# Kernel tuning notes

Hardware: AMD Instinct MI355X
Metric: run time of the kernel (lower is better)

The kernel has to match this reference:

```python
import jax, jax.numpy as jnp
import numpy as np

C = 64
CR = C // 8  # reduced channels for Q/K


def _conv1x1(x, W, b):
    # 1x1 conv == per-pixel linear over channels: x [b,c,h,w], W [o,c], b [o]
    return jnp.einsum('bchw,oc->bohw', x, W) + b[None, :, None, None]


def setup_inputs() -> dict:
    key = jax.random.key(0)
    ks = jax.random.split(key, 12)
    b, c, h, w = 8, C, 48, 48
    s = 1.0 / np.sqrt(c)
    inp = {
        'x1': jax.random.normal(ks[0], (b, c, h, w), jnp.float32),
        'x2': jax.random.normal(ks[1], (b, c, h, w), jnp.float32),
        'Wqk1': jax.random.normal(ks[2], (2 * CR, c), jnp.float32) * s,
        'bqk1': jnp.zeros((2 * CR,), jnp.float32),
        'Wqk2': jax.random.normal(ks[3], (2 * CR, c), jnp.float32) * s,
        'bqk2': jnp.zeros((2 * CR,), jnp.float32),
        'Wv1': jax.random.normal(ks[4], (c, c), jnp.float32) * s,
        'bv1': jnp.zeros((c,), jnp.float32),
        'Wv2': jax.random.normal(ks[5], (c, c), jnp.float32) * s,
        'bv2': jnp.zeros((c,), jnp.float32),
        'gamma': jnp.zeros((1,), jnp.float32) + 0.1,  # nonzero so output depends on attn
        'beta': jnp.zeros((1,), jnp.float32) + 0.1,
    }
    return inp


def reference(x1, x2, Wqk1, bqk1, Wqk2, bqk2, Wv1, bv1, Wv2, bv2, gamma, beta):
    b, c, h, w = x1.shape
    n = h * w
    qk1 = _conv1x1(x1, Wqk1, bqk1)
    qk2 = _conv1x1(x2, Wqk2, bqk2)
    q1, k1 = qk1[:, :CR], qk1[:, CR:]
    q2, k2 = qk2[:, :CR], qk2[:, CR:]
    # flatten spatial: [b, cr, n]
    q1 = q1.reshape(b, CR, n); k1 = k1.reshape(b, CR, n)
    q2 = q2.reshape(b, CR, n); k2 = k2.reshape(b, CR, n)
    v1 = _conv1x1(x1, Wv1, bv1).reshape(b, c, n)
    v2 = _conv1x1(x2, Wv2, bv2).reshape(b, c, n)
    # attn[b,i,j] = softmax_j( q[:, :, i] . k[:, :, j] )
    attn1 = jax.nn.softmax(jnp.einsum('bci,bcj->bij', q1, k1), axis=-1)
    attn2 = jax.nn.softmax(jnp.einsum('bci,bcj->bij', q2, k2), axis=-1)
    # out[:, :, j] = sum_i v[:, :, i] * attn[:, i, j]
    o1 = jnp.einsum('bci,bij->bcj', v1, attn2).reshape(b, c, h, w) * gamma + x1
    o2 = jnp.einsum('bci,bij->bcj', v2, attn1).reshape(b, c, h, w) * beta + x2
    return (o1, o2)
```

## Files before the change

kernel.cpp:

```cpp
#include <hip/hip_runtime.h>
#include <hip/hip_bf16.h>

#define NB   8
#define CCH  64
#define CR8  8
#define NPX  2304
#define BCN  (NB*CCH*NPX)
#define LOG2E 1.4426950408889634f

typedef short  short8   __attribute__((ext_vector_type(8)));
typedef unsigned short ushort4t __attribute__((ext_vector_type(4)));
typedef unsigned short ushort8t __attribute__((ext_vector_type(8)));
typedef float  float4t  __attribute__((ext_vector_type(4)));
typedef float  float16t __attribute__((ext_vector_type(16)));

static __device__ __forceinline__ unsigned short bf16bits(float f) {
    __hip_bfloat16 hb = __float2bfloat16(f);
    return *(unsigned short*)&hb;
}

#define WS_QB1 0
#define WS_KB1 (WS_QB1 + 147456)
#define WS_QB2 (WS_KB1 + 147456)
#define WS_KB2 (WS_QB2 + 147456)
#define WS_V1  (WS_KB2 + 147456)
#define WS_V2  (WS_V1 + BCN/2)
#define WS_PD  (WS_V2 + BCN/2)

__global__ __launch_bounds__(256) void proj_kernel(
    const float* __restrict__ x1, const float* __restrict__ x2,
    const float* __restrict__ Wqk1, const float* __restrict__ bqk1,
    const float* __restrict__ Wqk2, const float* __restrict__ bqk2,
    const float* __restrict__ Wv1,  const float* __restrict__ bv1,
    const float* __restrict__ Wv2,  const float* __restrict__ bv2,
    float* __restrict__ ws, float* __restrict__ out)
{
    const int t    = threadIdx.x;
    const int lane = t & 63;
    const int w    = t >> 6;
    const int n16  = lane & 15;
    const int c4   = lane >> 4;
    const int nt   = w & 1;
    const int mh   = w >> 1;
    const int b    = blockIdx.y;
    const int px   = blockIdx.x * 32 + nt * 16 + n16;

    const float* xsb[2];
    xsb[0] = x1 + ((size_t)b * CCH) * NPX + px;
    xsb[1] = x2 + ((size_t)b * CCH) * NPX + px;

    float xr[2][16];
    short8 bfrag[2][2];
    #pragma unroll
    for (int st = 0; st < 2; st++) {
        #pragma unroll
        for (int ch = 0; ch < 2; ch++) {
            #pragma unroll
            for (int j = 0; j < 8; j++)
                xr[st][ch * 8 + j] = xsb[st][(ch * 32 + c4 * 8 + j) * NPX];
            short8 f;
            #pragma unroll
            for (int j = 0; j < 8; j++)
                f[j] = (short)bf16bits(xr[st][ch * 8 + j]);
            bfrag[st][ch] = f;
        }
    }

    if (mh == 0) {
        #pragma unroll
        for (int st = 0; st < 2; st++) {
            float* outs = out + (st ? (size_t)BCN : 0);
            #pragma unroll
            for (int e = 0; e < 16; e++) {
                const int ch = (e >> 3) * 32 + c4 * 8 + (e & 7);
                outs[((size_t)b * CCH + ch) * NPX + px] = xr[st][e];
            }
        }
    }

    float4t acc[5];
    #pragma unroll
    for (int mt = 0; mt < 5; mt++) { acc[mt][0]=0.f; acc[mt][1]=0.f; acc[mt][2]=0.f; acc[mt][3]=0.f; }

    #pragma unroll
    for (int mt = 0; mt < 5; mt++) {
        const int mi  = mh * 5 + mt;
        const int isqk = (mi < 2);
        const int st  = isqk ? (mi & 1) : (mi >= 6);
        const float* Wb;
        int rowbase;
        if (isqk) { Wb = (mi == 0) ? Wqk1 : Wqk2; rowbase = 0; }
        else      { Wb = (mi >= 6) ? Wv2 : Wv1; rowbase = (mi - (mi >= 6 ? 6 : 2)) * 16; }
        const float* wrow = Wb + (size_t)(rowbase + n16) * 64 + c4 * 8;

        const short8 bf0 = st ? bfrag[1][0] : bfrag[0][0];
        const short8 bf1 = st ? bfrag[1][1] : bfrag[0][1];

        #pragma unroll
        for (int ch = 0; ch < 2; ch++) {
            const float4 a0 = *(const float4*)(wrow + ch * 32);
            const float4 a1 = *(const float4*)(wrow + ch * 32 + 4);
            short8 af;
            af[0] = (short)bf16bits(a0.x); af[1] = (short)bf16bits(a0.y);
            af[2] = (short)bf16bits(a0.z); af[3] = (short)bf16bits(a0.w);
            af[4] = (short)bf16bits(a1.x); af[5] = (short)bf16bits(a1.y);
            af[6] = (short)bf16bits(a1.z); af[7] = (short)bf16bits(a1.w);
            acc[mt] = __builtin_amdgcn_mfma_f32_16x16x32_bf16(
                af, ch ? bf1 : bf0, acc[mt], 0, 0, 0);
        }
    }

    #pragma unroll
    for (int mt = 0; mt < 5; mt++) {
        const int mi = mh * 5 + mt;
        if (mi < 2) {
            const int st = mi & 1;
            const float* bqk = st ? bqk2 : bqk1;
            unsigned short* qb = (unsigned short*)(ws + (st ? WS_QB2 : WS_QB1));
            unsigned short* kb = (unsigned short*)(ws + (st ? WS_KB2 : WS_KB1));
            const size_t rbase = (size_t)(b * NPX + px) * 16;
            #pragma unroll
            for (int r = 0; r < 4; r++) {
                const int oc = c4 * 4 + r;
                const float val = acc[mt][r] + bqk[oc];
                if (oc < 8)
                    qb[rbase + oc] = bf16bits(val * LOG2E);
                else
                    kb[rbase + (oc - 8)] = bf16bits(val);
            }
            ushort8t zq, zk;
            #pragma unroll
            for (int e = 0; e < 8; e++) { zq[e] = 0; zk[e] = 0; }
            zk[0] = 0x3F80; zk[1] = 0x3F80;
            if (c4 == 0) *(ushort8t*)(qb + rbase + 8) = zq;
            if (c4 == 2) *(ushort8t*)(kb + rbase + 8) = zk;
        } else {
            const int st = (mi >= 6);
            const int vt_ = mi - (st ? 6 : 2);
            const float* bv = st ? bv2 : bv1;
            unsigned short* v = (unsigned short*)(ws + (st ? WS_V2 : WS_V1));
            #pragma unroll
            for (int r = 0; r < 4; r++) {
                const int oc = vt_ * 16 + c4 * 4 + r;
                const float val = acc[mt][r] + bv[oc];
                v[((size_t)b * CCH + oc) * NPX + px] = bf16bits(val);
            }
        }
    }
}

__global__ __launch_bounds__(256) void stats_kernel(float* __restrict__ ws)
{
    const int t  = threadIdx.x;
    const int w  = t >> 6;
    const int n  = t & 31;
    const int h  = (t & 63) >> 5;
    const int jsb = blockIdx.x;
    const int iq  = blockIdx.y;
    const int ab  = blockIdx.z;
    const int b   = ab & 7;
    const int a   = ab >> 3;

    const unsigned short* qb = (const unsigned short*)(ws + (a ? WS_QB2 : WS_QB1));
    const unsigned short* kb = (const unsigned short*)(ws + (a ? WS_KB2 : WS_KB1));
    float* pd = ws + WS_PD;

    __shared__ float red[4][576];

    const int j = jsb * 128 + w * 32 + n;
    const short8 kfrag = *(const short8*)(kb + (size_t)(b * NPX + j) * 16 + h * 8);

    for (int ib = 0; ib < 18; ib++) {
        const int i = iq * 576 + ib * 32 + n;
        const short8 qfrag = *(const short8*)(qb + (size_t)(b * NPX + i) * 16 + h * 8);
        float16t acc = {};
        acc = __builtin_amdgcn_mfma_f32_32x32x16_bf16(kfrag, qfrag, acc, 0, 0, 0);
        float s0 = 0.f, s1 = 0.f, s2 = 0.f, s3 = 0.f;
        #pragma unroll
        for (int r = 0; r < 4; r++) {
            s0 += exp2f(acc[4 * r + 0]);
            s1 += exp2f(acc[4 * r + 1]);
            s2 += exp2f(acc[4 * r + 2]);
            s3 += exp2f(acc[4 * r + 3]);
        }
        float ssum = (s0 + s1) + (s2 + s3);
        ssum += __shfl_xor(ssum, 32);
        if (h == 0) red[w][ib * 32 + n] = ssum;
    }
    __syncthreads();
    for (int idx = t; idx < 576; idx += 256)
        pd[((size_t)ab * 18 + jsb) * NPX + iq * 576 + idx] =
            red[0][idx] + red[1][idx] + red[2][idx] + red[3][idx];
}

__global__ __launch_bounds__(256) void merge_fold(float* __restrict__ ws)
{
    const float* pd = ws + WS_PD;
    const int idx = blockIdx.x * 256 + threadIdx.x;
    const int i  = idx % NPX;
    const int ab = idx / NPX;
    const int b  = ab & 7;
    const int a  = ab >> 3;
    float d = 0.f;
    #pragma unroll
    for (int c = 0; c < 18; c++)
        d += pd[((size_t)ab * 18 + c) * NPX + i];
    const float m = -__log2f(d);

    const unsigned short mh = bf16bits(m);
    __hip_bfloat16 hb; *(unsigned short*)&hb = mh;
    const unsigned short ml = bf16bits(m - __bfloat162float(hb));

    unsigned short* qb = (unsigned short*)(ws + (a ? WS_QB2 : WS_QB1));
    const size_t rbase = (size_t)(b * NPX + i) * 16;
    qb[rbase + 8] = mh;
    qb[rbase + 9] = ml;
}

__global__ __launch_bounds__(256) void out_kernel(
    const float* __restrict__ gamma, const float* __restrict__ beta,
    const float* __restrict__ ws, float* __restrict__ out)
{
    const int t  = threadIdx.x;
    const int jt = blockIdx.x;
    const int b  = blockIdx.y;
    const int z  = blockIdx.z;
    const int o  = z >> 1;
    const int ihalf = z & 1;

    const int a = o ? 0 : 1;
    const unsigned short* qb = (const unsigned short*)(ws + (a ? WS_QB2 : WS_QB1));
    const unsigned short* kb = (const unsigned short*)(ws + (a ? WS_KB2 : WS_KB1));
    const unsigned short* v  = (const unsigned short*)(ws + (o ? WS_V2 : WS_V1));
    const float  scale = o ? beta[0] : gamma[0];

    __shared__ unsigned short vt[64][72];
    __shared__ unsigned short pt[64][132];

    const int j0   = jt * 64;
    const int lane = t & 63;
    const int w    = t >> 6;
    const int n    = lane & 31;
    const int h    = lane >> 5;
    const int jh   = w & 1;
    const int ihq  = w >> 1;
    const int cbase = 32 * (w & 1);
    const int jbase = 32 * (w >> 1);

    const short8 kfrag = *(const short8*)(kb + (size_t)(b * NPX + j0 + 32 * jh + n) * 16 + h * 8);

    float16t oacc = {};

    for (int it = 0; it < 18; it++) {
        const int i0 = ihalf * 1152 + it * 64;
        __syncthreads();

        #pragma unroll
        for (int r = 0; r < 2; r++) {
            const int seg = t + r * 256;
            const int c = seg >> 3, s8 = seg & 7;
            *(float4*)&vt[c][s8 * 8] =
                *(const float4*)(v + ((size_t)b * CCH + c) * NPX + i0 + s8 * 8);
        }

        const short8 qfrag = *(const short8*)(qb + (size_t)(b * NPX + i0 + 32 * ihq + n) * 16 + h * 8);
        float16t sc = {};
        sc = __builtin_amdgcn_mfma_f32_32x32x16_bf16(qfrag, kfrag, sc, 0, 0, 0);

        #pragma unroll
        for (int gq = 0; gq < 4; gq++) {
            const int ibl = 32 * ihq + 8 * gq + 4 * h;
            ushort4t pk;
            pk[0] = bf16bits(exp2f(sc[gq * 4 + 0]));
            pk[1] = bf16bits(exp2f(sc[gq * 4 + 1]));
            pk[2] = bf16bits(exp2f(sc[gq * 4 + 2]));
            pk[3] = bf16bits(exp2f(sc[gq * 4 + 3]));
            *(ushort4t*)&pt[32 * jh + n][ibl] = pk;
        }
        __syncthreads();

        #pragma unroll
        for (int kk = 0; kk < 4; kk++) {
            const short8 afrag = *(const short8*)&vt[cbase + n][kk * 16 + h * 8];
            const short8 bfrag = *(const short8*)&pt[jbase + n][kk * 16 + h * 8];
            oacc = __builtin_amdgcn_mfma_f32_32x32x16_bf16(afrag, bfrag, oacc, 0, 0, 0);
        }
    }

    const size_t outoff = o ? (size_t)BCN : 0;
    #pragma unroll
    for (int r = 0; r < 16; r++) {
        const int row = (r & 3) + 8 * (r >> 2) + 4 * h;
        const int c = cbase + row;
        const size_t gidx = ((size_t)b * CCH + c) * NPX + j0 + jbase + n;
        atomicAdd(&out[outoff + gidx], oacc[r] * scale);
    }
}

extern "C" void kernel_launch(void* const* d_in, const int* in_sizes, int n_in,
                              void* d_out, int out_size, void* d_ws, size_t ws_size,
                              hipStream_t stream)
{
    const float* x1   = (const float*)d_in[0];
    const float* x2   = (const float*)d_in[1];
    const float* Wqk1 = (const float*)d_in[2];
    const float* bqk1 = (const float*)d_in[3];
    const float* Wqk2 = (const float*)d_in[4];
    const float* bqk2 = (const float*)d_in[5];
    const float* Wv1  = (const float*)d_in[6];
    const float* bv1  = (const float*)d_in[7];
    const float* Wv2  = (const float*)d_in[8];
    const float* bv2  = (const float*)d_in[9];
    const float* gamma = (const float*)d_in[10];
    const float* beta  = (const float*)d_in[11];
    float* out = (float*)d_out;
    float* ws  = (float*)d_ws;

    proj_kernel<<<dim3(72, 8), 256, 0, stream>>>(
        x1, x2, Wqk1, bqk1, Wqk2, bqk2, Wv1, bv1, Wv2, bv2, ws, out);
    stats_kernel<<<dim3(18, 4, 16), 256, 0, stream>>>(ws);
    merge_fold<<<dim3(144), 256, 0, stream>>>(ws);
    out_kernel<<<dim3(36, 8, 4), 256, 0, stream>>>(gamma, beta, ws, out);
}
```

Measured before the change: 164.1 us.

## Prefetch next tiles in stats/out kernels and split out_kernel i-range into quarters

Software-pipelines the global loads in both stats_kernel (next Q fragment) and out_kernel (next V tile and Q fragment) into registers one iteration ahead, so load latency overlaps with MFMA and exp work. It also splits out_kernel's i-dimension into four chunks instead of two, doubling the grid to raise occupancy and parallelism on the many CUs. The cost is more atomicAdd traffic to the output and higher register pressure from the prefetch buffers.

After: 154.8 us. 5.6% less time.

```diff
diff --git a/kernel.cpp b/kernel.cpp
--- a/kernel.cpp
+++ b/kernel.cpp
@@ -170,11 +170,16 @@
     const int j = jsb * 128 + w * 32 + n;
     const short8 kfrag = *(const short8*)(kb + (size_t)(b * NPX + j) * 16 + h * 8);
 
+    short8 qf = *(const short8*)(qb + (size_t)(b * NPX + iq * 576 + n) * 16 + h * 8);
+
     for (int ib = 0; ib < 18; ib++) {
-        const int i = iq * 576 + ib * 32 + n;
-        const short8 qfrag = *(const short8*)(qb + (size_t)(b * NPX + i) * 16 + h * 8);
+        short8 qn = qf;
+        if (ib + 1 < 18) {
+            const int i = iq * 576 + (ib + 1) * 32 + n;
+            qn = *(const short8*)(qb + (size_t)(b * NPX + i) * 16 + h * 8);
+        }
         float16t acc = {};
-        acc = __builtin_amdgcn_mfma_f32_32x32x16_bf16(kfrag, qfrag, acc, 0, 0, 0);
+        acc = __builtin_amdgcn_mfma_f32_32x32x16_bf16(kfrag, qf, acc, 0, 0, 0);
         float s0 = 0.f, s1 = 0.f, s2 = 0.f, s3 = 0.f;
         #pragma unroll
         for (int r = 0; r < 4; r++) {
@@ -186,6 +191,7 @@
         float ssum = (s0 + s1) + (s2 + s3);
         ssum += __shfl_xor(ssum, 32);
         if (h == 0) red[w][ib * 32 + n] = ssum;
+        qf = qn;
     }
     __syncthreads();
     for (int idx = t; idx < 576; idx += 256)
@@ -225,8 +231,8 @@
     const int jt = blockIdx.x;
     const int b  = blockIdx.y;
     const int z  = blockIdx.z;
-    const int o  = z >> 1;
-    const int ihalf = z & 1;
+    const int o  = z >> 2;
+    const int ihalf = z & 3;
 
     const int a = o ? 0 : 1;
     const unsigned short* qb = (const unsigned short*)(ws + (a ? WS_QB2 : WS_QB1));
@@ -249,23 +255,35 @@
 
     const short8 kfrag = *(const short8*)(kb + (size_t)(b * NPX + j0 + 32 * jh + n) * 16 + h * 8);
 
+    const int c0 = t >> 3, s80 = (t & 7) * 8;
+    const int c1 = (t + 256) >> 3, s81 = ((t + 256) & 7) * 8;
+
+    const int ibase = ihalf * 576;
+    float4 vpre0 = *(const float4*)(v + ((size_t)b * CCH + c0) * NPX + ibase + s80);
+    float4 vpre1 = *(const float4*)(v + ((size_t)b * CCH + c1) * NPX + ibase + s81);
+    short8 qpre  = *(const short8*)(qb + (size_t)(b * NPX + ibase + 32 * ihq + n) * 16 + h * 8);
+
     float16t oacc = {};
 
-    for (int it = 0; it < 18; it++) {
-        const int i0 = ihalf * 1152 + it * 64;
+    for (int it = 0; it < 9; it++) {
+        const int i0 = ibase + it * 64;
+
+        float4 vn0 = vpre0, vn1 = vpre1;
+        short8 qn = qpre;
+        if (it + 1 < 9) {
+            const int i0n = i0 + 64;
+            vn0 = *(const float4*)(v + ((size_t)b * CCH + c0) * NPX + i0n + s80);
+            vn1 = *(const float4*)(v + ((size_t)b * CCH + c1) * NPX + i0n + s81);
+            qn  = *(const short8*)(qb + (size_t)(b * NPX + i0n + 32 * ihq + n) * 16 + h * 8);
+        }
+
         __syncthreads();
 
-        #pragma unroll
-        for (int r = 0; r < 2; r++) {
-            const int seg = t + r * 256;
-            const int c = seg >> 3, s8 = seg & 7;
-            *(float4*)&vt[c][s8 * 8] =
-                *(const float4*)(v + ((size_t)b * CCH + c) * NPX + i0 + s8 * 8);
-        }
-
-        const short8 qfrag = *(const short8*)(qb + (size_t)(b * NPX + i0 + 32 * ihq + n) * 16 + h * 8);
+        *(float4*)&vt[c0][s80] = vpre0;
+        *(float4*)&vt[c1][s81] = vpre1;
+
         float16t sc = {};
-        sc = __builtin_amdgcn_mfma_f32_32x32x16_bf16(qfrag, kfrag, sc, 0, 0, 0);
+        sc = __builtin_amdgcn_mfma_f32_32x32x16_bf16(qpre, kfrag, sc, 0, 0, 0);
 
         #pragma unroll
         for (int gq = 0; gq < 4; gq++) {
@@ -285,6 +303,8 @@
             const short8 bfrag = *(const short8*)&pt[jbase + n][kk * 16 + h * 8];
             oacc = __builtin_amdgcn_mfma_f32_32x32x16_bf16(afrag, bfrag, oacc, 0, 0, 0);
         }
+
+        vpre0 = vn0; vpre1 = vn1; qpre = qn;
     }
 
     const size_t outoff = o ? (size_t)BCN : 0;
@@ -320,5 +340,5 @@
         x1, x2, Wqk1, bqk1, Wqk2, bqk2, Wv1, bv1, Wv2, bv2, ws, out);
     stats_kernel<<<dim3(18, 4, 16), 256, 0, stream>>>(ws);
     merge_fold<<<dim3(144), 256, 0, stream>>>(ws);
-    out_kernel<<<dim3(36, 8, 4), 256, 0, stream>>>(gamma, beta, ws, out);
-}
+    out_kernel<<<dim3(36, 8, 8), 256, 0, stream>>>(gamma, beta, ws, out);
+}
```
